# Kernel optimization log

Measured on AMD Instinct MI355X. Metric: run time of the kernel, lower is better.

The kernel has to match this reference:

```python
import jax, jax.numpy as jnp
import numpy as np

N, E, G, H = 50000, 800000, 2048, 128
DIS = 3  # dis_emb is None -> raw frac_diff (3 dims)
EIN = 2 * H + 6 + DIS  # 265


def _lin_init(key, fan_in, fan_out):
    lim = 1.0 / np.sqrt(fan_in)
    return jax.random.uniform(key, (fan_in, fan_out), jnp.float32, -lim, lim)


def setup_inputs() -> dict:
    key = jax.random.key(0)
    ks = jax.random.split(key, 12)
    node_features = jax.random.normal(ks[0], (N, H), jnp.float32)
    frac_coords = jax.random.uniform(ks[1], (N, 3), jnp.float32)
    lattices = jax.random.normal(ks[2], (G, 6), jnp.float32)
    frac_diff = jax.random.normal(ks[3], (E, 3), jnp.float32)
    edge_index = jax.random.randint(ks[4], (2, E), 0, N, jnp.int64 if jax.config.jax_enable_x64 else jnp.int32)
    edge2graph = jax.random.randint(ks[5], (E,), 0, G, edge_index.dtype)
    return dict(
        node_features=node_features,
        frac_coords=frac_coords,
        lattices=lattices,
        frac_diff=frac_diff,
        edge_index=edge_index,
        edge2graph=edge2graph,
        e_w1=_lin_init(ks[6], EIN, H), e_b1=jnp.zeros((H,), jnp.float32),
        e_w2=_lin_init(ks[7], H, H), e_b2=jnp.zeros((H,), jnp.float32),
        n_w1=_lin_init(ks[8], 2 * H, H), n_b1=jnp.zeros((H,), jnp.float32),
        n_w2=_lin_init(ks[9], H, H), n_b2=jnp.zeros((H,), jnp.float32),
    )


def reference(node_features, frac_coords, lattices, frac_diff, edge_index, edge2graph,
              e_w1, e_b1, e_w2, e_b2, n_w1, n_b1, n_w2, n_b2):
    n_nodes = node_features.shape[0]
    silu = jax.nn.silu
    # edge model: gather endpoints, concat with per-graph lattice + frac_diff
    hi = node_features[edge_index[0]]            # [E, H]
    hj = node_features[edge_index[1]]            # [E, H]
    lat = lattices[edge2graph]                   # [E, 6]
    edges_input = jnp.concatenate([hi, hj, lat, frac_diff], axis=1)  # [E, 265]
    e = silu(edges_input @ e_w1 + e_b1)
    edge_features = silu(e @ e_w2 + e_b2)        # [E, H]
    # scatter-mean aggregate onto source nodes
    seg = edge_index[0]
    agg_sum = jax.ops.segment_sum(edge_features, seg, num_segments=n_nodes)
    cnt = jax.ops.segment_sum(jnp.ones((edge_features.shape[0],), edge_features.dtype), seg, num_segments=n_nodes)
    agg = agg_sum / jnp.maximum(cnt, 1.0)[:, None]
    # node model + residual
    h = jnp.concatenate([node_features, agg], axis=1)  # [N, 2H]
    h = silu(h @ n_w1 + n_b1)
    node_output = silu(h @ n_w2 + n_b2)
    return node_features + node_output
```

## Files before the change

kernel.cpp:

```cpp
#include <hip/hip_runtime.h>

#define N_NODES 50000
#define N_EDGES 800000
#define HDIM 128
#define N_GRAPH 2048

typedef __bf16 bf16x8 __attribute__((ext_vector_type(8)));
typedef float f32x4 __attribute__((ext_vector_type(4)));
typedef float f32x16 __attribute__((ext_vector_type(16)));

static __device__ __forceinline__ unsigned short f2bf(float f) {
    unsigned int u = __float_as_uint(f);
    u += 0x7fffu + ((u >> 16) & 1u);
    return (unsigned short)(u >> 16);
}
static __device__ __forceinline__ float bflo(unsigned int u) { return __uint_as_float(u << 16); }
static __device__ __forceinline__ float bfhi(unsigned int u) { return __uint_as_float(u & 0xFFFF0000u); }

static __device__ __forceinline__ unsigned int cvt_pk_bf16(float lo, float hi) {
    unsigned int r;
    asm("v_cvt_pk_bf16_f32 %0, %1, %2" : "=v"(r) : "v"(lo), "v"(hi));
    return r;
}

static __device__ __forceinline__ float silu_f(float x) {
    float e = __builtin_amdgcn_exp2f(x * -1.44269504f);
    return x * __builtin_amdgcn_rcpf(1.0f + e);
}

#define PREP_BLOCKS 1408
#define HIST_BLOCKS 3125
#define ZERO_BLOCKS 6250
__global__ void prep_hist_kernel(const float* __restrict__ ew1, const float* __restrict__ ew2,
                                 const float* __restrict__ nw1, const float* __restrict__ nw2,
                                 const float* __restrict__ eb1, const float* __restrict__ lattices,
                                 const int* __restrict__ eidx,
                                 unsigned short* __restrict__ W1aT, unsigned short* __restrict__ W1bT,
                                 unsigned short* __restrict__ W2t, unsigned short* __restrict__ N1t,
                                 unsigned short* __restrict__ N2t, unsigned short* __restrict__ Lb,
                                 int* __restrict__ buf, float* __restrict__ agg) {
    const int bid = blockIdx.x;
    if (bid >= PREP_BLOCKS + HIST_BLOCKS) {
        const int idx = (bid - PREP_BLOCKS - HIST_BLOCKS) * 256 + threadIdx.x;
        ((float4*)agg)[idx] = make_float4(0.f, 0.f, 0.f, 0.f);
        return;
    }
    if (bid >= PREP_BLOCKS) {
        int e = (bid - PREP_BLOCKS) * 256 + threadIdx.x;
        if (e < N_EDGES) atomicAdd(&buf[eidx[e]], 1);
        return;
    }
    int i = bid * 256 + threadIdx.x;
    if (i < 16384) {
        int n = i >> 7, k = i & 127;
        W1aT[i] = f2bf(ew1[k * 128 + n]);
    } else if (i < 32768) {
        int j = i - 16384; int n = j >> 7, k = j & 127;
        W1bT[j] = f2bf(ew1[(128 + k) * 128 + n]);
    } else if (i < 49152) {
        int j = i - 32768; int n = j >> 7, k = j & 127;
        W2t[j] = f2bf(ew2[k * 128 + n]);
    } else if (i < 81920) {
        int j = i - 49152; int n = j >> 8, k = j & 255;
        N1t[j] = f2bf(nw1[k * 128 + n]);
    } else if (i < 98304) {
        int j = i - 81920; int n = j >> 7, k = j & 127;
        N2t[j] = f2bf(nw2[k * 128 + n]);
    } else if (i < 98304 + 262144) {
        int j = i - 98304; int g = j >> 7, c = j & 127;
        float s = eb1[c];
#pragma unroll
        for (int t = 0; t < 6; ++t) s += lattices[g * 6 + t] * ew1[(256 + t) * 128 + c];
        Lb[j] = f2bf(s);
    }
}

__global__ __launch_bounds__(1024) void scan_kernel(int* __restrict__ buf) {
    constexpr int CH = 12288;
    __shared__ int lds[CH];
    __shared__ int wpart[16];
    __shared__ int carry_s;
    const int t = threadIdx.x;
    const int wave = t >> 6, lane = t & 63;
    if (t == 0) carry_s = 0;
    __syncthreads();
#pragma unroll 1
    for (int base = 0; base < N_NODES; base += CH) {
#pragma unroll
        for (int k = 0; k < CH / 1024; ++k) {
            int f = k * 1024 + t;
            lds[f] = (base + f < N_NODES) ? buf[base + f] : 0;
        }
        __syncthreads();
        int loc[12];
        int s = 0;
#pragma unroll
        for (int i = 0; i < 12; ++i) { loc[i] = lds[t * 12 + i]; s += loc[i]; }
        int ps = s;
#pragma unroll
        for (int off = 1; off < 64; off <<= 1) {
            int v = __shfl_up(ps, off);
            if (lane >= off) ps += v;
        }
        if (lane == 63) wpart[wave] = ps;
        __syncthreads();
        if (t == 0) {
            int r = carry_s;
#pragma unroll
            for (int i = 0; i < 16; ++i) { int v = wpart[i]; wpart[i] = r; r += v; }
            carry_s = r;
        }
        __syncthreads();
        int run = wpart[wave] + (ps - s);
#pragma unroll
        for (int i = 0; i < 12; ++i) { int tmp = loc[i]; lds[t * 12 + i] = run; run += tmp; }
        __syncthreads();
#pragma unroll
        for (int k = 0; k < CH / 1024; ++k) {
            int f = k * 1024 + t;
            if (base + f < N_NODES) buf[base + f] = lds[f];
        }
        __syncthreads();
    }
}

#define PERM_BLOCKS2 3125
#define PQ_BLOCKS ((N_NODES + 63) / 64)
__global__ __launch_bounds__(256, 4) void perm_pq_kernel(
    const int* __restrict__ eidx, const int* __restrict__ e2g,
    const float* __restrict__ frac_diff, int* __restrict__ buf,
    unsigned short* __restrict__ perm_lo, unsigned char* __restrict__ perm_hi,
    uint4* __restrict__ rec, const int packed,
    const float* __restrict__ nf, const unsigned short* __restrict__ W1aT,
    const unsigned short* __restrict__ W1bT,
    unsigned short* __restrict__ P, unsigned short* __restrict__ Qm) {
    constexpr int SA = 136;
    __shared__ unsigned short sm[64 * SA];
    const int bid = blockIdx.x;
    const int tid = threadIdx.x;

    if (bid < PERM_BLOCKS2) {
        int e = bid * 256 + tid;
        if (e < N_EDGES) {
            int s = eidx[e];
            int pos = atomicAdd(&buf[s], 1);
            if (packed) {
                int d = eidx[N_EDGES + e];
                int g = e2g[e];
                unsigned int w0 = (unsigned int)s | ((unsigned int)d << 16);
                unsigned int w1 = (unsigned int)g | ((unsigned int)f2bf(frac_diff[3 * e]) << 16);
                unsigned int w2 = (unsigned int)f2bf(frac_diff[3 * e + 1]) |
                                  ((unsigned int)f2bf(frac_diff[3 * e + 2]) << 16);
                rec[pos] = make_uint4(w0, w1, w2, 0u);
            } else {
                perm_lo[pos] = (unsigned short)(e & 0xFFFF);
                perm_hi[pos] = (unsigned char)(e >> 16);
            }
        }
        return;
    }

    const int n0 = (bid - PERM_BLOCKS2) * 64;
    const int mrow = tid >> 2, q = tid & 3;
    {
        const int node = n0 + mrow;
        unsigned short* row = sm + mrow * SA + q * 32;
        if (node < N_NODES) {
            const float4* a4 = (const float4*)(nf + (size_t)node * HDIM) + q * 8;
#pragma unroll
            for (int j = 0; j < 8; ++j) {
                float4 v = a4[j];
                *(ushort4*)(row + 4 * j) = make_ushort4(f2bf(v.x), f2bf(v.y), f2bf(v.z), f2bf(v.w));
            }
        } else {
#pragma unroll
            for (int j = 0; j < 8; ++j) *(ushort4*)(row + 4 * j) = make_ushort4(0, 0, 0, 0);
        }
    }
    __syncthreads();

    const int wave = tid >> 6, lane = tid & 63;
    const int lr = lane & 15, kq = lane >> 4;
    f32x4 acca[8] = {}, accb[8] = {};
    const int arow = (wave * 16 + lr) * SA;
#pragma unroll
    for (int ks = 0; ks < 128; ks += 32) {
        bf16x8 a = *(const bf16x8*)(sm + arow + ks + kq * 8);
#pragma unroll
        for (int nt = 0; nt < 8; ++nt) {
            bf16x8 ba = *(const bf16x8*)(W1aT + (nt * 16 + lr) * 128 + ks + kq * 8);
            acca[nt] = __builtin_amdgcn_mfma_f32_16x16x32_bf16(a, ba, acca[nt], 0, 0, 0);
            bf16x8 bb = *(const bf16x8*)(W1bT + (nt * 16 + lr) * 128 + ks + kq * 8);
            accb[nt] = __builtin_amdgcn_mfma_f32_16x16x32_bf16(a, bb, accb[nt], 0, 0, 0);
        }
    }
    __syncthreads();

    const int node = n0 + mrow;
#pragma unroll
    for (int nt = 0; nt < 8; ++nt) {
        const int col = nt * 16 + lr;
#pragma unroll
        for (int r = 0; r < 4; ++r)
            sm[(wave * 16 + kq * 4 + r) * SA + col] = f2bf(acca[nt][r]);
    }
    __syncthreads();
    if (node < N_NODES) {
        uint4* dst = (uint4*)(P + (size_t)node * HDIM + q * 32);
        const uint4* srcp = (const uint4*)(sm + mrow * SA + q * 32);
#pragma unroll
        for (int j = 0; j < 4; ++j) dst[j] = srcp[j];
    }
    __syncthreads();
#pragma unroll
    for (int nt = 0; nt < 8; ++nt) {
        const int col = nt * 16 + lr;
#pragma unroll
        for (int r = 0; r < 4; ++r)
            sm[(wave * 16 + kq * 4 + r) * SA + col] = f2bf(accb[nt][r]);
    }
    __syncthreads();
    if (node < N_NODES) {
        uint4* dst = (uint4*)(Qm + (size_t)node * HDIM + q * 32);
        const uint4* srcp = (const uint4*)(sm + mrow * SA + q * 32);
#pragma unroll
        for (int j = 0; j < 4; ++j) dst[j] = srcp[j];
    }
}


static __device__ __forceinline__ void build_afrag(
    const uint4* pu, const uint4* qu, const uint4* lu,
    float f0, float f1, float f2,
    const unsigned int* wlds, int hi, bf16x8* afrag) {
#pragma unroll
    for (int kk = 0; kk < 8; ++kk) {
        const unsigned int* wl = wlds + (kk * 2 + hi) * 12;
        const uint4 w0v = *(const uint4*)(wl);
        const uint4 w1v = *(const uint4*)(wl + 4);
        const uint4 w2v = *(const uint4*)(wl + 8);
        const unsigned int* pw = (const unsigned int*)&pu[kk];
        const unsigned int* qw = (const unsigned int*)&qu[kk];
        const unsigned int* lw = (const unsigned int*)&lu[kk];
        const unsigned int* w0w = (const unsigned int*)&w0v;
        const unsigned int* w1w = (const unsigned int*)&w1v;
        const unsigned int* w2w = (const unsigned int*)&w2v;
        unsigned int ow[4];
#pragma unroll
        for (int w = 0; w < 4; ++w) {
            float x0 = bflo(pw[w]) + bflo(qw[w]) + bflo(lw[w])
                     + f0 * bflo(w0w[w]) + f1 * bflo(w1w[w]) + f2 * bflo(w2w[w]);
            float x1 = bfhi(pw[w]) + bfhi(qw[w]) + bfhi(lw[w])
                     + f0 * bfhi(w0w[w]) + f1 * bfhi(w1w[w]) + f2 * bfhi(w2w[w]);
            ow[w] = cvt_pk_bf16(silu_f(x0), silu_f(x1));
        }
        afrag[kk] = *(bf16x8*)ow;
    }
}

static __device__ __forceinline__ void do_mfma(
    const bf16x8* afrag, const unsigned short* __restrict__ W2t,
    int row, int hi, f32x16* acc) {
    __builtin_amdgcn_s_setprio(1);
#pragma unroll
    for (int kk = 0; kk < 8; ++kk) {
#pragma unroll
        for (int t4 = 0; t4 < 4; ++t4) {
            bf16x8 bb = *(const bf16x8*)(W2t + (t4 * 32 + row) * 128 + kk * 16 + hi * 8);
            acc[t4] = __builtin_amdgcn_mfma_f32_32x32x16_bf16(afrag[kk], bb, acc[t4], 0, 0, 0);
        }
    }
    __builtin_amdgcn_s_setprio(0);
}

static __device__ __forceinline__ void epilogue(
    const f32x16* acc, const int* sc, const int* snq,
    int row, int hi, const float* __restrict__ b2, float* __restrict__ agg) {
#pragma unroll
    for (int t4 = 0; t4 < 4; ++t4) {
        const int col = t4 * 32 + row;
        const float bias = b2[col];
        float p[16], tq[4], to[4];
#pragma unroll
        for (int rq = 0; rq < 4; ++rq) {
            float s0 = silu_f(acc[t4][4 * rq + 0] + bias);
            float s1 = silu_f(acc[t4][4 * rq + 1] + bias);
            float s2 = silu_f(acc[t4][4 * rq + 2] + bias);
            float s3 = silu_f(acc[t4][4 * rq + 3] + bias);
            p[4 * rq + 0] = s0;
            p[4 * rq + 1] = s0 + s1;
            p[4 * rq + 2] = p[4 * rq + 1] + s2;
            p[4 * rq + 3] = p[4 * rq + 2] + s3;
            tq[rq] = p[4 * rq + 3];
            to[rq] = __shfl_xor(tq[rq], 32);
        }
        float cum = 0.f;
#pragma unroll
        for (int rq = 0; rq < 4; ++rq) {
            const float off = cum + (hi ? to[rq] : 0.f);
            cum += tq[rq] + to[rq];
#pragma unroll
            for (int i = 0; i < 4; ++i) {
                const int r = 4 * rq + i;
                const float val = p[r] + off;
                const int myrow = 4 * (2 * rq + hi) + i;
                const bool lastg = (myrow == 31);
                const int nxt = (i < 3) ? sc[r + 1] : snq[rq];
                const bool bnd = lastg || (sc[r] != nxt);
                if (bnd) {
                    atomicAdd(&agg[(size_t)sc[r] * HDIM + col], val);
                    if (!lastg) atomicAdd(&agg[(size_t)nxt * HDIM + col], -val);
                }
            }
        }
    }
}

#define EDGE_NWG (N_EDGES / 256)
template <bool PACKED>
static __device__ __forceinline__ void fetch_meta(
    int i, const uint4* __restrict__ rec, const int* __restrict__ eidx,
    const int* __restrict__ e2g, const float* __restrict__ frac_diff,
    const unsigned short* __restrict__ perm_lo, const unsigned char* __restrict__ perm_hi,
    int& src, int& dst, int& g, float& f0, float& f1, float& f2) {
    if (PACKED) {
        const uint4 rv = rec[i];
        src = rv.x & 0xFFFF;
        dst = rv.x >> 16;
        g = rv.y & 0xFFFF;
        f0 = bfhi(rv.y);
        f1 = bflo(rv.z);
        f2 = bfhi(rv.z);
    } else {
        const int e = (int)perm_lo[i] | ((int)perm_hi[i] << 16);
        src = eidx[e];
        dst = eidx[N_EDGES + e];
        g = e2g[e];
        f0 = frac_diff[3 * e];
        f1 = frac_diff[3 * e + 1];
        f2 = frac_diff[3 * e + 2];
    }
}

static __device__ __forceinline__ void gather_rows(
    const unsigned short* __restrict__ P, const unsigned short* __restrict__ Qm,
    const unsigned short* __restrict__ Lb,
    int src, int dst, int g, int hi, uint4* pu, uint4* qu, uint4* lu) {
    const size_t pr = (size_t)src * HDIM, qr = (size_t)dst * HDIM, lr = (size_t)g * HDIM;
#pragma unroll
    for (int kk = 0; kk < 8; ++kk) {
        const int c0 = kk * 16 + hi * 8;
        pu[kk] = *(const uint4*)(P + pr + c0);
        qu[kk] = *(const uint4*)(Qm + qr + c0);
        lu[kk] = *(const uint4*)(Lb + lr + c0);
    }
}

static __device__ __forceinline__ void make_sc(int src, int hi, int* sc, int* snq) {
#pragma unroll
    for (int r = 0; r < 16; ++r) sc[r] = __shfl(src, (r & 3) + 8 * (r >> 2) + 4 * hi);
#pragma unroll
    for (int j = 0; j < 4; ++j) snq[j] = __shfl(src, (4 * (2 * j + hi) + 4) & 31);
}

template <bool PACKED>
__global__ __launch_bounds__(256, 2) void edge_kernel(
    const unsigned short* __restrict__ P, const unsigned short* __restrict__ Qm,
    const unsigned short* __restrict__ Lb, const float* __restrict__ frac_diff,
    const int* __restrict__ eidx, const int* __restrict__ e2g,
    const unsigned short* __restrict__ perm_lo, const unsigned char* __restrict__ perm_hi,
    const uint4* __restrict__ rec,
    const float* __restrict__ e_w1, const unsigned short* __restrict__ W2t,
    const float* __restrict__ b2, float* __restrict__ agg) {
    __shared__ __align__(16) unsigned int wlds[192];
    const int tid = threadIdx.x;
    {
        const float* wrbase = e_w1 + 262 * HDIM;
        if (tid < 192) {
            const int w = tid & 3, rw = (tid >> 2) % 3, hi = (tid / 12) & 1, kk = tid / 24;
            const int c = kk * 16 + hi * 8 + 2 * w;
            wlds[((kk * 2 + hi) * 3 + rw) * 4 + w] =
                (unsigned int)f2bf(wrbase[rw * HDIM + c]) |
                ((unsigned int)f2bf(wrbase[rw * HDIM + c + 1]) << 16);
        }
    }
    __syncthreads();

    const int wv = tid >> 6, lane = tid & 63;
    const int row = lane & 31, hi = lane >> 5;
    const int base = (blockIdx.x * 4 + wv) * 64;

    int srcA, dstA, gA; float fA0, fA1, fA2;
    fetch_meta<PACKED>(base + row, rec, eidx, e2g, frac_diff, perm_lo, perm_hi,
                       srcA, dstA, gA, fA0, fA1, fA2);
    int srcB, dstB, gB; float fB0, fB1, fB2;
    fetch_meta<PACKED>(base + 32 + row, rec, eidx, e2g, frac_diff, perm_lo, perm_hi,
                       srcB, dstB, gB, fB0, fB1, fB2);

    uint4 puA[8], quA[8], luA[8];
    gather_rows(P, Qm, Lb, srcA, dstA, gA, hi, puA, quA, luA);
    uint4 puB[8], quB[8], luB[8];
    gather_rows(P, Qm, Lb, srcB, dstB, gB, hi, puB, quB, luB);

    {
        bf16x8 afrag[8];
        build_afrag(puA, quA, luA, fA0, fA1, fA2, wlds, hi, afrag);
        int sc[16], snq[4];
        make_sc(srcA, hi, sc, snq);
        f32x16 acc[4] = {};
        do_mfma(afrag, W2t, row, hi, acc);
        epilogue(acc, sc, snq, row, hi, b2, agg);
    }

    {
        bf16x8 afrag[8];
        build_afrag(puB, quB, luB, fB0, fB1, fB2, wlds, hi, afrag);
        int sc[16], snq[4];
        make_sc(srcB, hi, sc, snq);
        f32x16 acc[4] = {};
        do_mfma(afrag, W2t, row, hi, acc);
        epilogue(acc, sc, snq, row, hi, b2, agg);
    }
}

__global__ __launch_bounds__(256, 4) void node_kernel(
    const float* __restrict__ nf, const float* __restrict__ agg,
    const int* __restrict__ buf,
    const unsigned short* __restrict__ N1t, const float* __restrict__ b1,
    const unsigned short* __restrict__ N2t, const float* __restrict__ b2,
    float* __restrict__ out) {
    constexpr int SA = 264;
    constexpr int S2 = 136;
    constexpr int SFo = 132;
    __shared__ unsigned short sm[64 * SA];
    float* smf = (float*)sm;

    const int tid = threadIdx.x;
    const int n0 = blockIdx.x * 64;
    const int mrow = tid >> 2, q = tid & 3;
    {
        const int node = n0 + mrow;
        unsigned short* row = sm + mrow * SA;
        const int cbq = q * 32;
        if (node < N_NODES) {
            const int c = buf[node] - (node ? buf[node - 1] : 0);
            const float inv = 1.0f / (float)max(c, 1);
            const float4* a4 = (const float4*)(nf + (size_t)node * HDIM) + q * 8;
            const float4* g4 = (const float4*)(agg + (size_t)node * HDIM) + q * 8;
#pragma unroll
            for (int j = 0; j < 8; ++j) {
                float4 v = a4[j];
                *(ushort4*)(row + cbq + 4 * j) =
                    make_ushort4(f2bf(v.x), f2bf(v.y), f2bf(v.z), f2bf(v.w));
                float4 g = g4[j];
                *(ushort4*)(row + HDIM + cbq + 4 * j) =
                    make_ushort4(f2bf(g.x * inv), f2bf(g.y * inv), f2bf(g.z * inv), f2bf(g.w * inv));
            }
        } else {
#pragma unroll
            for (int j = 0; j < 8; ++j) {
                *(ushort4*)(row + cbq + 4 * j) = make_ushort4(0, 0, 0, 0);
                *(ushort4*)(row + HDIM + cbq + 4 * j) = make_ushort4(0, 0, 0, 0);
            }
        }
    }
    __syncthreads();

    const int wave = tid >> 6, lane = tid & 63;
    const int lr = lane & 15, kq = lane >> 4;

    f32x4 acc[8] = {};
    const int arow = (wave * 16 + lr) * SA;
#pragma unroll
    for (int ks = 0; ks < 256; ks += 32) {
        bf16x8 a = *(const bf16x8*)(sm + arow + ks + kq * 8);
#pragma unroll
        for (int nt = 0; nt < 8; ++nt) {
            bf16x8 bb = *(const bf16x8*)(N1t + (nt * 16 + lr) * 256 + ks + kq * 8);
            acc[nt] = __builtin_amdgcn_mfma_f32_16x16x32_bf16(a, bb, acc[nt], 0, 0, 0);
        }
    }
    __syncthreads();

#pragma unroll
    for (int nt = 0; nt < 8; ++nt) {
        const int col = nt * 16 + lr;
        const float bias = b1[col];
#pragma unroll
        for (int r = 0; r < 4; ++r) {
            const int mm = wave * 16 + kq * 4 + r;
            sm[mm * S2 + col] = f2bf(silu_f(acc[nt][r] + bias));
        }
    }
    __syncthreads();

    f32x4 acc2[8] = {};
    const int arow2 = (wave * 16 + lr) * S2;
#pragma unroll
    for (int ks = 0; ks < 128; ks += 32) {
        bf16x8 a = *(const bf16x8*)(sm + arow2 + ks + kq * 8);
#pragma unroll
        for (int nt = 0; nt < 8; ++nt) {
            bf16x8 bb = *(const bf16x8*)(N2t + (nt * 16 + lr) * 128 + ks + kq * 8);
            acc2[nt] = __builtin_amdgcn_mfma_f32_16x16x32_bf16(a, bb, acc2[nt], 0, 0, 0);
        }
    }
    __syncthreads();

#pragma unroll
    for (int nt = 0; nt < 8; ++nt) {
        const int col = nt * 16 + lr;
        const float bias = b2[col];
#pragma unroll
        for (int r = 0; r < 4; ++r) {
            const int mm = wave * 16 + kq * 4 + r;
            smf[mm * SFo + col] = silu_f(acc2[nt][r] + bias);
        }
    }
    __syncthreads();
    {
        const int node = n0 + mrow;
        if (node < N_NODES) {
            const float4* nfr = (const float4*)(nf + (size_t)node * HDIM) + q * 8;
            float4* outr = (float4*)(out + (size_t)node * HDIM) + q * 8;
            const float* st = smf + mrow * SFo + q * 32;
#pragma unroll
            for (int j = 0; j < 8; ++j) {
                float4 v = nfr[j];
                float4 s4 = *(const float4*)(st + 4 * j);
                v.x += s4.x; v.y += s4.y; v.z += s4.z; v.w += s4.w;
                outr[j] = v;
            }
        }
    }
}

extern "C" void kernel_launch(void* const* d_in, const int* in_sizes, int n_in,
                              void* d_out, int out_size, void* d_ws, size_t ws_size,
                              hipStream_t stream) {
    const float* node_features = (const float*)d_in[0];
    const float* lattices = (const float*)d_in[2];
    const float* frac_diff = (const float*)d_in[3];
    const int* edge_index = (const int*)d_in[4];
    const int* edge2graph = (const int*)d_in[5];
    const float* e_w1 = (const float*)d_in[6];
    const float* e_b1 = (const float*)d_in[7];
    const float* e_w2 = (const float*)d_in[8];
    const float* e_b2 = (const float*)d_in[9];
    const float* n_w1 = (const float*)d_in[10];
    const float* n_b1 = (const float*)d_in[11];
    const float* n_w2 = (const float*)d_in[12];
    const float* n_b2 = (const float*)d_in[13];

    char* ws = (char*)d_ws;
    unsigned short* W1aT = (unsigned short*)(ws);
    unsigned short* W1bT = (unsigned short*)(ws + 32768);
    unsigned short* W2t  = (unsigned short*)(ws + 65536);
    unsigned short* N1t  = (unsigned short*)(ws + 98304);
    unsigned short* N2t  = (unsigned short*)(ws + 163840);
    unsigned short* Lb   = (unsigned short*)(ws + 196608);
    unsigned short* P    = (unsigned short*)(ws + 720896);
    unsigned short* Qm   = (unsigned short*)(ws + 13520896);
    int* buf             = (int*)(ws + 26320896);
    unsigned short* perm_lo = (unsigned short*)(ws + 26520896);
    unsigned char* perm_hi  = (unsigned char*)(ws + 28120896);
    uint4* rec           = (uint4*)(ws + 28920896);
    float* agg = (float*)d_out;

    const int packed = (ws_size >= 28920896 + (size_t)N_EDGES * 16) ? 1 : 0;

    hipMemsetAsync(buf, 0, (size_t)N_NODES * 4, stream);

    prep_hist_kernel<<<PREP_BLOCKS + HIST_BLOCKS + ZERO_BLOCKS, 256, 0, stream>>>(
        e_w1, e_w2, n_w1, n_w2, e_b1, lattices, edge_index,
        W1aT, W1bT, W2t, N1t, N2t, Lb, buf, agg);

    scan_kernel<<<1, 1024, 0, stream>>>(buf);

    perm_pq_kernel<<<PERM_BLOCKS2 + PQ_BLOCKS, 256, 0, stream>>>(
        edge_index, edge2graph, frac_diff, buf, perm_lo, perm_hi, rec, packed,
        node_features, W1aT, W1bT, P, Qm);

    if (packed) {
        edge_kernel<true><<<EDGE_NWG, 256, 0, stream>>>(
            P, Qm, Lb, frac_diff, edge_index, edge2graph, perm_lo, perm_hi, rec,
            e_w1, W2t, e_b2, agg);
    } else {
        edge_kernel<false><<<EDGE_NWG, 256, 0, stream>>>(
            P, Qm, Lb, frac_diff, edge_index, edge2graph, perm_lo, perm_hi, rec,
            e_w1, W2t, e_b2, agg);
    }

    node_kernel<<<(N_NODES + 63) / 64, 256, 0, stream>>>(
        node_features, agg, buf, N1t, n_b1, N2t, n_b2, (float*)d_out);
}
```

Baseline: 536.9 us.

## Overlap serial prefix scan with P/Q node GEMM; split permutation into own kernel

The single-block exclusive scan over node degrees now runs as block 0 of the P/Q projection kernel, so the other blocks compute node projections while the scan proceeds. The scan uses a 256-thread block with 4096-element chunks instead of 1024 threads. The edge permutation and packing moves into a separate kernel launched after the scan, since it needs the scanned offsets. The s_setprio hints around the edge MFMA loop are also removed. The scan itself runs with fewer threads and may be slower, and there is still the same number of launches.

```diff
diff --git a/kernel.cpp b/kernel.cpp
--- a/kernel.cpp
+++ b/kernel.cpp
@@ -75,92 +75,67 @@
     }
 }
 
-__global__ __launch_bounds__(1024) void scan_kernel(int* __restrict__ buf) {
-    constexpr int CH = 12288;
-    __shared__ int lds[CH];
-    __shared__ int wpart[16];
-    __shared__ int carry_s;
-    const int t = threadIdx.x;
-    const int wave = t >> 6, lane = t & 63;
-    if (t == 0) carry_s = 0;
-    __syncthreads();
-#pragma unroll 1
-    for (int base = 0; base < N_NODES; base += CH) {
-#pragma unroll
-        for (int k = 0; k < CH / 1024; ++k) {
-            int f = k * 1024 + t;
-            lds[f] = (base + f < N_NODES) ? buf[base + f] : 0;
-        }
-        __syncthreads();
-        int loc[12];
-        int s = 0;
-#pragma unroll
-        for (int i = 0; i < 12; ++i) { loc[i] = lds[t * 12 + i]; s += loc[i]; }
-        int ps = s;
-#pragma unroll
-        for (int off = 1; off < 64; off <<= 1) {
-            int v = __shfl_up(ps, off);
-            if (lane >= off) ps += v;
-        }
-        if (lane == 63) wpart[wave] = ps;
-        __syncthreads();
-        if (t == 0) {
-            int r = carry_s;
-#pragma unroll
-            for (int i = 0; i < 16; ++i) { int v = wpart[i]; wpart[i] = r; r += v; }
-            carry_s = r;
-        }
-        __syncthreads();
-        int run = wpart[wave] + (ps - s);
-#pragma unroll
-        for (int i = 0; i < 12; ++i) { int tmp = loc[i]; lds[t * 12 + i] = run; run += tmp; }
-        __syncthreads();
-#pragma unroll
-        for (int k = 0; k < CH / 1024; ++k) {
-            int f = k * 1024 + t;
-            if (base + f < N_NODES) buf[base + f] = lds[f];
-        }
-        __syncthreads();
-    }
-}
-
-#define PERM_BLOCKS2 3125
 #define PQ_BLOCKS ((N_NODES + 63) / 64)
-__global__ __launch_bounds__(256, 4) void perm_pq_kernel(
-    const int* __restrict__ eidx, const int* __restrict__ e2g,
-    const float* __restrict__ frac_diff, int* __restrict__ buf,
-    unsigned short* __restrict__ perm_lo, unsigned char* __restrict__ perm_hi,
-    uint4* __restrict__ rec, const int packed,
+__global__ __launch_bounds__(256, 4) void scan_pq_kernel(
+    int* __restrict__ buf,
     const float* __restrict__ nf, const unsigned short* __restrict__ W1aT,
     const unsigned short* __restrict__ W1bT,
     unsigned short* __restrict__ P, unsigned short* __restrict__ Qm) {
     constexpr int SA = 136;
     __shared__ unsigned short sm[64 * SA];
+    constexpr int CH = 4096;
+    __shared__ int slds[CH];
+    __shared__ int wpart[4];
+    __shared__ int carry_s;
     const int bid = blockIdx.x;
     const int tid = threadIdx.x;
 
-    if (bid < PERM_BLOCKS2) {
-        int e = bid * 256 + tid;
-        if (e < N_EDGES) {
-            int s = eidx[e];
-            int pos = atomicAdd(&buf[s], 1);
-            if (packed) {
-                int d = eidx[N_EDGES + e];
-                int g = e2g[e];
-                unsigned int w0 = (unsigned int)s | ((unsigned int)d << 16);
-                unsigned int w1 = (unsigned int)g | ((unsigned int)f2bf(frac_diff[3 * e]) << 16);
-                unsigned int w2 = (unsigned int)f2bf(frac_diff[3 * e + 1]) |
-                                  ((unsigned int)f2bf(frac_diff[3 * e + 2]) << 16);
-                rec[pos] = make_uint4(w0, w1, w2, 0u);
-            } else {
-                perm_lo[pos] = (unsigned short)(e & 0xFFFF);
-                perm_hi[pos] = (unsigned char)(e >> 16);
-            }
+    if (bid == 0) {
+        const int wave = tid >> 6, lane = tid & 63;
+        if (tid == 0) carry_s = 0;
+        __syncthreads();
+#pragma unroll 1
+        for (int base = 0; base < N_NODES; base += CH) {
+#pragma unroll
+            for (int k = 0; k < CH / 256; ++k) {
+                int f = k * 256 + tid;
+                slds[f] = (base + f < N_NODES) ? buf[base + f] : 0;
+            }
+            __syncthreads();
+            int loc[16];
+            int s = 0;
+#pragma unroll
+            for (int i = 0; i < 16; ++i) { loc[i] = slds[tid * 16 + i]; s += loc[i]; }
+            int ps = s;
+#pragma unroll
+            for (int off = 1; off < 64; off <<= 1) {
+                int v = __shfl_up(ps, off);
+                if (lane >= off) ps += v;
+            }
+            if (lane == 63) wpart[wave] = ps;
+            __syncthreads();
+            if (tid == 0) {
+                int r = carry_s;
+#pragma unroll
+                for (int i = 0; i < 4; ++i) { int v = wpart[i]; wpart[i] = r; r += v; }
+                carry_s = r;
+            }
+            __syncthreads();
+            int run = wpart[wave] + (ps - s);
+#pragma unroll
+            for (int i = 0; i < 16; ++i) { int tmp = loc[i]; slds[tid * 16 + i] = run; run += tmp; }
+            __syncthreads();
+#pragma unroll
+            for (int k = 0; k < CH / 256; ++k) {
+                int f = k * 256 + tid;
+                if (base + f < N_NODES) buf[base + f] = slds[f];
+            }
+            __syncthreads();
         }
         return;
     }
 
-    const int n0 = (bid - PERM_BLOCKS2) * 64;
+    const int n0 = (bid - 1) * 64;
     const int mrow = tid >> 2, q = tid & 3;
     {
         const int node = n0 + mrow;
@@ -225,6 +200,31 @@
         const uint4* srcp = (const uint4*)(sm + mrow * SA + q * 32);
 #pragma unroll
         for (int j = 0; j < 4; ++j) dst[j] = srcp[j];
+    }
+}
+
+#define PERM_BLOCKS2 3125
+__global__ __launch_bounds__(256, 4) void perm_kernel(
+    const int* __restrict__ eidx, const int* __restrict__ e2g,
+    const float* __restrict__ frac_diff, int* __restrict__ buf,
+    unsigned short* __restrict__ perm_lo, unsigned char* __restrict__ perm_hi,
+    uint4* __restrict__ rec, const int packed) {
+    int e = blockIdx.x * 256 + threadIdx.x;
+    if (e < N_EDGES) {
+        int s = eidx[e];
+        int pos = atomicAdd(&buf[s], 1);
+        if (packed) {
+            int d = eidx[N_EDGES + e];
+            int g = e2g[e];
+            unsigned int w0 = (unsigned int)s | ((unsigned int)d << 16);
+            unsigned int w1 = (unsigned int)g | ((unsigned int)f2bf(frac_diff[3 * e]) << 16);
+            unsigned int w2 = (unsigned int)f2bf(frac_diff[3 * e + 1]) |
+                              ((unsigned int)f2bf(frac_diff[3 * e + 2]) << 16);
+            rec[pos] = make_uint4(w0, w1, w2, 0u);
+        } else {
+            perm_lo[pos] = (unsigned short)(e & 0xFFFF);
+            perm_hi[pos] = (unsigned char)(e >> 16);
+        }
     }
 }
 
@@ -261,7 +261,6 @@
 static __device__ __forceinline__ void do_mfma(
     const bf16x8* afrag, const unsigned short* __restrict__ W2t,
     int row, int hi, f32x16* acc) {
-    __builtin_amdgcn_s_setprio(1);
 #pragma unroll
     for (int kk = 0; kk < 8; ++kk) {
 #pragma unroll
@@ -270,7 +269,6 @@
             acc[t4] = __builtin_amdgcn_mfma_f32_32x32x16_bf16(afrag[kk], bb, acc[t4], 0, 0, 0);
         }
     }
-    __builtin_amdgcn_s_setprio(0);
 }
 
 static __device__ __forceinline__ void epilogue(
@@ -575,11 +573,11 @@
         e_w1, e_w2, n_w1, n_w2, e_b1, lattices, edge_index,
         W1aT, W1bT, W2t, N1t, N2t, Lb, buf, agg);
 
-    scan_kernel<<<1, 1024, 0, stream>>>(buf);
-
-    perm_pq_kernel<<<PERM_BLOCKS2 + PQ_BLOCKS, 256, 0, stream>>>(
-        edge_index, edge2graph, frac_diff, buf, perm_lo, perm_hi, rec, packed,
-        node_features, W1aT, W1bT, P, Qm);
+    scan_pq_kernel<<<1 + PQ_BLOCKS, 256, 0, stream>>>(
+        buf, node_features, W1aT, W1bT, P, Qm);
+
+    perm_kernel<<<PERM_BLOCKS2, 256, 0, stream>>>(
+        edge_index, edge2graph, frac_diff, buf, perm_lo, perm_hi, rec, packed);
 
     if (packed) {
         edge_kernel<true><<<EDGE_NWG, 256, 0, stream>>>(
```

Measured after the change: 534.8 us. Within noise of the previous version (-0.4%).
